# Optimization experiments

Hardware: AMD Instinct MI355X
Metric: run time of the kernel (lower is better)

## Reference

```python
import jax, jax.numpy as jnp
import numpy as np

B = 8           # hardcoded batchsize in the original forward
EPS = 1e-4      # scn.BatchNormalization default eps


def setup_inputs() -> dict:
    key = jax.random.key(0)
    ks = jax.random.split(key, 8)
    Nq, Nkv = 16384, 32768
    dec_in, enc_in, nf = 64, 64, 128
    nbr = jax.random.randint(ks[2], (Nq, 27), 0, Nq, dtype=jnp.int32)
    # center tap of the 3x3x3 submanifold conv is the point itself
    nbr = nbr.at[:, 13].set(jnp.arange(Nq, dtype=jnp.int32))
    return {
        "x_decoder_feat": jax.random.normal(ks[0], (Nq, dec_in), jnp.float32),
        "x_encoder_feat": jax.random.normal(ks[1], (Nkv, enc_in), jnp.float32),
        "nbr_idx": nbr,
        "W_p1": jax.random.normal(ks[3], (27, dec_in, nf), jnp.float32) * 0.05,
        "W_q": jax.random.normal(ks[4], (nf, nf), jnp.float32) * 0.05,
        "W_k": jax.random.normal(ks[5], (enc_in, nf), jnp.float32) * 0.05,
        "W_v": jax.random.normal(ks[6], (enc_in, nf), jnp.float32) * 0.05,
        "W_trans": jax.random.normal(ks[7], (nf, nf), jnp.float32) * 0.05,
        "gamma": jnp.ones((nf,), jnp.float32),
        "beta": jnp.zeros((nf,), jnp.float32),
    }


def reference(x_decoder_feat, x_encoder_feat, nbr_idx, W_p1, W_q, W_k, W_v,
              W_trans, gamma, beta):
    nf = W_q.shape[1]
    # p1: 3x3x3 submanifold conv = gather 27 neighbors, per-offset matmul, sum
    x_dec = jnp.einsum('nkc,kcf->nf', x_decoder_feat[nbr_idx], W_p1)  # [Nq,nf]
    q = (x_dec @ W_q).reshape(B, -1, nf)            # [B, nq, nf]
    k = (x_encoder_feat @ W_k).reshape(B, -1, nf)   # [B, nkv, nf]
    v = (x_encoder_feat @ W_v).reshape(B, -1, nf)
    # per-batch QK^T softmax V (no 1/sqrt(d) scaling in original)
    attn = jax.nn.softmax(jnp.einsum('bqc,bkc->bqk', q, k), axis=-1)
    x_r = jnp.einsum('bqk,bkc->bqc', attn, v).reshape(-1, nf)  # [Nq,nf]
    # trans_conv (1x1) + batchnorm (batch stats over all points)
    t = x_r @ W_trans
    mean = t.mean(axis=0)
    var = t.var(axis=0)
    bn = (t - mean) * jax.lax.rsqrt(var + EPS) * gamma + beta
    return x_dec + bn
```

## Files before the change

### kernel.cpp

```cpp
#include <hip/hip_runtime.h>
#include <math.h>

#define NQ      16384
#define NKV     32768
#define CIN     64
#define NF      128
#define NOFF    27
#define BATCH   8
#define SQ      2048
#define SKV     4096
#define BN_EPS  1e-4f
#define SPLIT   4
#define KV_PER_SPLIT (SKV / SPLIT)
#define TILES_PER_SPLIT (KV_PER_SPLIT / 64)
#define LOG2E   1.4426950408889634f
#define SHIFT2  57.70780163555854f

typedef unsigned short u16;
typedef unsigned int   u32;
typedef __attribute__((ext_vector_type(4))) float f32x4;
typedef __attribute__((ext_vector_type(8))) short s16x8;

__device__ __forceinline__ u16 f2b(float x) {
    union { float f; unsigned u; } c; c.f = x;
    unsigned r = (c.u + 0x7FFFu + ((c.u >> 16) & 1u)) >> 16;
    return (u16)r;
}
__device__ __forceinline__ float b2f(u16 x) {
    union { unsigned u; float f; } c; c.u = ((unsigned)x) << 16;
    return c.f;
}
__device__ __forceinline__ u32 pk2bf(float lo, float hi) {
    union { float f; u32 u; } a, b;
    a.f = lo; b.f = hi;
    return __builtin_amdgcn_perm(b.u + 0x8000u, a.u + 0x8000u, 0x07060302u);
}
__device__ __forceinline__ void g2l16(const void* gp, void* lp) {
    __builtin_amdgcn_global_load_lds(
        (const __attribute__((address_space(1))) unsigned*)gp,
        (__attribute__((address_space(3))) unsigned*)lp, 16, 0, 0);
}

__device__ __forceinline__ void wtrans_one(
    const float* __restrict__ src, u16* __restrict__ dst, int K, int id, float sc)
{
    int n  = id / (K / 4);
    int k4 = (id % (K / 4)) * 4;
    const float* s = src + (size_t)k4 * NF + n;
    ushort4 o;
    o.x = f2b(s[0] * sc); o.y = f2b(s[NF] * sc);
    o.z = f2b(s[2 * NF] * sc); o.w = f2b(s[3 * NF] * sc);
    *(ushort4*)(dst + (size_t)n * K + k4) = o;
}

__global__ __launch_bounds__(256) void prep_kernel(
    const float* __restrict__ xdec_feat, const float* __restrict__ Wp1,
    const float* __restrict__ Wq, const float* __restrict__ Wk,
    const float* __restrict__ Wv, const float* __restrict__ Wt,
    u16* __restrict__ xf_bf, u16* __restrict__ wp1t,
    u16* __restrict__ wqT, u16* __restrict__ wkT,
    u16* __restrict__ wvT, u16* __restrict__ wtT,
    float* __restrict__ stats)
{
    int bid = blockIdx.x;
    int t   = threadIdx.x;
    if (bid < 1024) {
        int i = (bid * 256 + t) * 4;
        float4 v = *(const float4*)(xdec_feat + i);
        ushort4 o;
        o.x = f2b(v.x); o.y = f2b(v.y); o.z = f2b(v.z); o.w = f2b(v.w);
        *(ushort4*)(xf_bf + i) = o;
    } else if (bid < 1240) {
        int id = (bid - 1024) * 256 + t;
        int ko = id >> 11;
        int r  = id & 2047;
        int f  = r >> 4;
        int c4 = (r & 15) * 4;
        const float* s = Wp1 + (size_t)ko * 8192 + (size_t)c4 * NF + f;
        ushort4 o;
        o.x = f2b(s[0]); o.y = f2b(s[NF]); o.z = f2b(s[2 * NF]); o.w = f2b(s[3 * NF]);
        *(ushort4*)(wp1t + (size_t)ko * 8192 + (size_t)f * 64 + c4) = o;
    } else if (bid < 1288) {
        int id = (bid - 1240) * 256 + t;
        if (id < 4096)        wtrans_one(Wq, wqT, 128, id, LOG2E);
        else if (id < 6144)   wtrans_one(Wk, wkT, 64, id - 4096, 1.f);
        else if (id < 8192)   wtrans_one(Wv, wvT, 64, id - 6144, 1.f);
        else                  wtrans_one(Wt, wtT, 128, id - 8192, 1.f);
    } else {
        stats[t] = 0.f;
    }
}

__global__ __launch_bounds__(256) void main_fused_kernel(
    const float* __restrict__ xenc, const u16* __restrict__ xf,
    const int* __restrict__ nbr, const u16* __restrict__ wp1t,
    const u16* __restrict__ wqT, const u16* __restrict__ wkT,
    const u16* __restrict__ wvT,
    u16* __restrict__ kbuf, u16* __restrict__ vt,
    float* __restrict__ xdec, u16* __restrict__ qbuf)
{
    __shared__ u16 Bs[2][128][64];
    __shared__ int nbr_s[64][28];

    const int t    = threadIdx.x;
    const int w    = t >> 6;
    const int lane = t & 63;
    const int quad = lane >> 4;
    const int l15  = lane & 15;

    if (blockIdx.x < 512) {
        const int m0 = blockIdx.x * 64 + w * 16;
        const float* Ap = xenc + (size_t)(m0 + l15) * CIN + quad * 8;
        float4 a0 = *(const float4*)(Ap);
        float4 a1 = *(const float4*)(Ap + 4);
        float4 a2 = *(const float4*)(Ap + 32);
        float4 a3 = *(const float4*)(Ap + 36);
        union { u16 a[8]; s16x8 v; } p0, p1;
        p0.a[0] = f2b(a0.x); p0.a[1] = f2b(a0.y); p0.a[2] = f2b(a0.z); p0.a[3] = f2b(a0.w);
        p0.a[4] = f2b(a1.x); p0.a[5] = f2b(a1.y); p0.a[6] = f2b(a1.z); p0.a[7] = f2b(a1.w);
        p1.a[0] = f2b(a2.x); p1.a[1] = f2b(a2.y); p1.a[2] = f2b(a2.z); p1.a[3] = f2b(a2.w);
        p1.a[4] = f2b(a3.x); p1.a[5] = f2b(a3.y); p1.a[6] = f2b(a3.z); p1.a[7] = f2b(a3.w);
        s16x8 af0 = p0.v, af1 = p1.v;

        int m  = m0 + quad * 4;
        int bb = m >> 12;
        int kv = m & 4095;
        #pragma unroll
        for (int nt = 0; nt < 8; nt++) {
            f32x4 ka = (f32x4)0.f, va = (f32x4)0.f;
            const u16* Kp = wkT + (size_t)(nt * 16 + l15) * CIN + quad * 8;
            const u16* Vp = wvT + (size_t)(nt * 16 + l15) * CIN + quad * 8;
            s16x8 kb0 = *(const s16x8*)(Kp);
            s16x8 kb1 = *(const s16x8*)(Kp + 32);
            s16x8 vb0 = *(const s16x8*)(Vp);
            s16x8 vb1 = *(const s16x8*)(Vp + 32);
            ka = __builtin_amdgcn_mfma_f32_16x16x32_bf16(af0, kb0, ka, 0, 0, 0);
            ka = __builtin_amdgcn_mfma_f32_16x16x32_bf16(af1, kb1, ka, 0, 0, 0);
            va = __builtin_amdgcn_mfma_f32_16x16x32_bf16(af0, vb0, va, 0, 0, 0);
            va = __builtin_amdgcn_mfma_f32_16x16x32_bf16(af1, vb1, va, 0, 0, 0);
            #pragma unroll
            for (int r = 0; r < 4; r++)
                kbuf[(size_t)(m0 + quad * 4 + r) * NF + nt * 16 + l15] = f2b(ka[r]);
            ushort4 pk;
            pk.x = f2b(va[0]); pk.y = f2b(va[1]); pk.z = f2b(va[2]); pk.w = f2b(va[3]);
            *(ushort4*)(vt + (size_t)(bb * NF + nt * 16 + l15) * SKV + kv) = pk;
        }
        return;
    }

    const int base = (blockIdx.x - 512) * 64;

    for (int i = t; i < 64 * NOFF; i += 256)
        nbr_s[i / NOFF][i % NOFF] = nbr[(size_t)base * NOFF + i];

    f32x4 oacc[8];
    #pragma unroll
    for (int n = 0; n < 8; n++) oacc[n] = (f32x4)0.f;

    const int arow = w * 16 + l15;
    const int sr   = w * 32 + (lane >> 3);

    #pragma unroll
    for (int c = 0; c < 4; c++) {
        int row = sr + c * 8;
        int kk  = (lane & 7) ^ (row & 7);
        g2l16(wp1t + (size_t)row * 64 + kk * 8, &Bs[0][w * 32 + c * 8][0]);
    }
    __syncthreads();

    for (int ko = 0; ko < NOFF; ko++) {
        int cur = ko & 1;
        if (ko + 1 < NOFF) {
            int nxt = (ko + 1) & 1;
            #pragma unroll
            for (int c = 0; c < 4; c++) {
                int row = sr + c * 8;
                int kk  = (lane & 7) ^ (row & 7);
                g2l16(wp1t + (size_t)(ko + 1) * 8192 + (size_t)row * 64 + kk * 8,
                      &Bs[nxt][w * 32 + c * 8][0]);
            }
        }
        int nb = nbr_s[arow][ko];
        const u16* ap = xf + (size_t)nb * CIN + quad * 8;
        s16x8 af0 = *(const s16x8*)(ap);
        s16x8 af1 = *(const s16x8*)(ap + 32);
        #pragma unroll
        for (int nt = 0; nt < 8; nt++) {
            int pc0 = quad ^ (l15 & 7);
            int pc1 = (4 + quad) ^ (l15 & 7);
            s16x8 bf0 = *(const s16x8*)&Bs[cur][nt * 16 + l15][pc0 * 8];
            s16x8 bf1 = *(const s16x8*)&Bs[cur][nt * 16 + l15][pc1 * 8];
            oacc[nt] = __builtin_amdgcn_mfma_f32_16x16x32_bf16(af0, bf0, oacc[nt], 0, 0, 0);
            oacc[nt] = __builtin_amdgcn_mfma_f32_16x16x32_bf16(af1, bf1, oacc[nt], 0, 0, 0);
        }
        __syncthreads();
    }

    u16* xq = &Bs[0][0][0];
    #pragma unroll
    for (int nt = 0; nt < 8; nt++)
        #pragma unroll
        for (int r = 0; r < 4; r++) {
            int row = w * 16 + quad * 4 + r;
            int col = nt * 16 + l15;
            xdec[(size_t)(base + row) * NF + col] = oacc[nt][r];
            xq[row * 136 + col] = f2b(oacc[nt][r]);
        }

    s16x8 aq[4];
    #pragma unroll
    for (int ks = 0; ks < 4; ks++)
        aq[ks] = *(const s16x8*)&xq[(w * 16 + l15) * 136 + ks * 32 + quad * 8];

    #pragma unroll
    for (int nt = 0; nt < 8; nt++) {
        f32x4 acc = (f32x4)0.f;
        const u16* Wp = wqT + (size_t)(nt * 16 + l15) * NF + quad * 8;
        #pragma unroll
        for (int ks = 0; ks < 4; ks++) {
            s16x8 bf = *(const s16x8*)(Wp + ks * 32);
            acc = __builtin_amdgcn_mfma_f32_16x16x32_bf16(aq[ks], bf, acc, 0, 0, 0);
        }
        #pragma unroll
        for (int r = 0; r < 4; r++)
            qbuf[(size_t)(base + w * 16 + quad * 4 + r) * NF + nt * 16 + l15] = f2b(acc[r]);
    }
}

__global__ __launch_bounds__(256) void attn_mfma_kernel(
    const u16* __restrict__ Q, const u16* __restrict__ K,
    const u16* __restrict__ Vt, u16* __restrict__ Opart,
    float* __restrict__ lpart)
{
    __shared__ u16 Ks[2][64][128];
    __shared__ u16 Vs[2][128][64];
    __shared__ u16 Ps[4][16][72];

    const int t    = threadIdx.x;
    const int b    = blockIdx.y;
    const int q0   = blockIdx.x * 128;
    const int sp   = blockIdx.z;
    const int w    = t >> 6;
    const int lane = t & 63;
    const int quad = lane >> 4;
    const int l15  = lane & 15;

    const u16* Kb  = K  + (size_t)b * SKV * NF;
    const u16* Vtb = Vt + (size_t)b * NF * SKV;

    s16x8 qf[2][4];
    #pragma unroll
    for (int g = 0; g < 2; g++) {
        const u16* Qp = Q + ((size_t)(b * SQ + q0 + w * 32 + g * 16 + l15)) * NF + quad * 8;
        #pragma unroll
        for (int ks = 0; ks < 4; ks++) qf[g][ks] = *(const s16x8*)(Qp + ks * 32);
    }

    f32x4 oacc[2][8];
    #pragma unroll
    for (int g = 0; g < 2; g++)
        #pragma unroll
        for (int n = 0; n < 8; n++) oacc[g][n] = (f32x4)0.f;
    float lrow[2] = {0.f, 0.f};

    const int kvbase = sp * KV_PER_SPLIT;
    const int krow = w * 16 + (lane >> 4);
    const int vrow = w * 32 + (lane >> 3);

    #pragma unroll
    for (int c = 0; c < 4; c++) {
        int row = krow + c * 4;
        int k8  = (lane & 15) ^ (row & 15);
        g2l16(Kb + (size_t)(kvbase + row) * NF + k8 * 8, &Ks[0][w * 16 + c * 4][0]);
    }
    #pragma unroll
    for (int c = 0; c < 4; c++) {
        int row = vrow + c * 8;
        int k8  = (lane & 7) ^ (row & 7);
        g2l16(Vtb + (size_t)row * SKV + kvbase + k8 * 8, &Vs[0][w * 32 + c * 8][0]);
    }

    for (int tile = 0; tile < TILES_PER_SPLIT; tile++) {
        const int cur = tile & 1;
        __syncthreads();
        if (tile + 1 < TILES_PER_SPLIT) {
            const int nxt = (tile + 1) & 1;
            int kvn = kvbase + (tile + 1) * 64;
            #pragma unroll
            for (int c = 0; c < 4; c++) {
                int row = krow + c * 4;
                int k8  = (lane & 15) ^ (row & 15);
                g2l16(Kb + (size_t)(kvn + row) * NF + k8 * 8, &Ks[nxt][w * 16 + c * 4][0]);
            }
            #pragma unroll
            for (int c = 0; c < 4; c++) {
                int row = vrow + c * 8;
                int k8  = (lane & 7) ^ (row & 7);
                g2l16(Vtb + (size_t)row * SKV + kvn + k8 * 8, &Vs[nxt][w * 32 + c * 8][0]);
            }
        }

        f32x4 sacc[2][4];
        #pragma unroll
        for (int c = 0; c < 4; c++) {
            sacc[0][c] = (f32x4)0.f;
            sacc[1][c] = (f32x4)0.f;
            #pragma unroll
            for (int ks = 0; ks < 4; ks++) {
                int p = (ks * 4 + quad) ^ l15;
                s16x8 ka = *(const s16x8*)&Ks[cur][c * 16 + l15][p * 8];
                sacc[0][c] = __builtin_amdgcn_mfma_f32_16x16x32_bf16(ka, qf[0][ks], sacc[0][c], 0, 0, 0);
                sacc[1][c] = __builtin_amdgcn_mfma_f32_16x16x32_bf16(ka, qf[1][ks], sacc[1][c], 0, 0, 0);
            }
        }

        s16x8 pb[2][2];
        #pragma unroll
        for (int g = 0; g < 2; g++) {
            float rs = 0.f;
            float pv[4][4];
            #pragma unroll
            for (int c = 0; c < 4; c++)
                #pragma unroll
                for (int r = 0; r < 4; r++) {
                    float p = exp2f(sacc[g][c][r] - SHIFT2);
                    pv[c][r] = p;
                    rs += p;
                }
            rs += __shfl_xor(rs, 16);
            rs += __shfl_xor(rs, 32);
            lrow[g] += rs;
            #pragma unroll
            for (int c = 0; c < 4; c++) {
                uint2 pk;
                pk.x = pk2bf(pv[c][0], pv[c][1]);
                pk.y = pk2bf(pv[c][2], pv[c][3]);
                *(uint2*)&Ps[w][l15][c * 16 + quad * 4] = pk;
            }
            pb[g][0] = *(const s16x8*)&Ps[w][l15][quad * 8];
            pb[g][1] = *(const s16x8*)&Ps[w][l15][32 + quad * 8];
        }

        #pragma unroll
        for (int mt = 0; mt < 8; mt++) {
            int p0 = quad ^ (l15 & 7);
            int p1 = (4 + quad) ^ (l15 & 7);
            s16x8 va0 = *(const s16x8*)&Vs[cur][mt * 16 + l15][p0 * 8];
            s16x8 va1 = *(const s16x8*)&Vs[cur][mt * 16 + l15][p1 * 8];
            oacc[0][mt] = __builtin_amdgcn_mfma_f32_16x16x32_bf16(va0, pb[0][0], oacc[0][mt], 0, 0, 0);
            oacc[0][mt] = __builtin_amdgcn_mfma_f32_16x16x32_bf16(va1, pb[0][1], oacc[0][mt], 0, 0, 0);
            oacc[1][mt] = __builtin_amdgcn_mfma_f32_16x16x32_bf16(va0, pb[1][0], oacc[1][mt], 0, 0, 0);
            oacc[1][mt] = __builtin_amdgcn_mfma_f32_16x16x32_bf16(va1, pb[1][1], oacc[1][mt], 0, 0, 0);
        }
    }

    #pragma unroll
    for (int g = 0; g < 2; g++) {
        int grow = b * SQ + q0 + w * 32 + g * 16 + l15;
        u16* Ob = Opart + (size_t)sp * NQ * NF + (size_t)grow * NF;
        #pragma unroll
        for (int mt = 0; mt < 8; mt++) {
            uint2 ov;
            ov.x = pk2bf(oacc[g][mt][0], oacc[g][mt][1]);
            ov.y = pk2bf(oacc[g][mt][2], oacc[g][mt][3]);
            *(uint2*)(Ob + mt * 16 + quad * 4) = ov;
        }
        if (quad == 0) lpart[sp * NQ + grow] = lrow[g];
    }
}

__global__ __launch_bounds__(256) void tgemm_fused_kernel(
    const u16* __restrict__ Opart, const float* __restrict__ lpart,
    const u16* __restrict__ WT, float* __restrict__ C, float* __restrict__ stats)
{
    const int t    = threadIdx.x;
    const int w    = t >> 6;
    const int lane = t & 63;
    const int quad = lane >> 4;
    const int l15  = lane & 15;
    const int m0   = blockIdx.x * 64 + w * 16;
    const int row  = m0 + l15;

    float L = 0.f;
    #pragma unroll
    for (int s = 0; s < SPLIT; s++) L += lpart[s * NQ + row];
    float invL = 1.f / L;

    s16x8 af[4];
    #pragma unroll
    for (int ks = 0; ks < 4; ks++) {
        float sum[8] = {0.f, 0.f, 0.f, 0.f, 0.f, 0.f, 0.f, 0.f};
        #pragma unroll
        for (int s = 0; s < SPLIT; s++) {
            const u16* p = Opart + (size_t)s * NQ * NF + (size_t)row * NF + ks * 32 + quad * 8;
            ushort4 u0 = *(const ushort4*)p;
            ushort4 u1 = *(const ushort4*)(p + 4);
            sum[0] += b2f(u0.x); sum[1] += b2f(u0.y);
            sum[2] += b2f(u0.z); sum[3] += b2f(u0.w);
            sum[4] += b2f(u1.x); sum[5] += b2f(u1.y);
            sum[6] += b2f(u1.z); sum[7] += b2f(u1.w);
        }
        union { u16 a[8]; s16x8 v; } pk;
        #pragma unroll
        for (int j = 0; j < 8; j++) pk.a[j] = f2b(sum[j] * invL);
        af[ks] = pk.v;
    }

    f32x4 oacc[8];
    #pragma unroll
    for (int nt = 0; nt < 8; nt++) {
        oacc[nt] = (f32x4)0.f;
        const u16* Wp = WT + (size_t)(nt * 16 + l15) * NF + quad * 8;
        #pragma unroll
        for (int ks = 0; ks < 4; ks++) {
            s16x8 bf = *(const s16x8*)(Wp + ks * 32);
            oacc[nt] = __builtin_amdgcn_mfma_f32_16x16x32_bf16(af[ks], bf, oacc[nt], 0, 0, 0);
        }
    }

    float s[8], sq[8];
    #pragma unroll
    for (int nt = 0; nt < 8; nt++) {
        s[nt] = 0.f; sq[nt] = 0.f;
        #pragma unroll
        for (int r = 0; r < 4; r++) {
            float v = oacc[nt][r];
            C[(size_t)(m0 + quad * 4 + r) * NF + nt * 16 + l15] = v;
            s[nt] += v; sq[nt] += v * v;
        }
    }
    #pragma unroll
    for (int nt = 0; nt < 8; nt++) {
        s[nt]  += __shfl_xor(s[nt], 16);  s[nt]  += __shfl_xor(s[nt], 32);
        sq[nt] += __shfl_xor(sq[nt], 16); sq[nt] += __shfl_xor(sq[nt], 32);
    }
    __shared__ float red[2][4][128];
    if (quad == 0) {
        #pragma unroll
        for (int nt = 0; nt < 8; nt++) {
            red[0][w][nt * 16 + l15] = s[nt];
            red[1][w][nt * 16 + l15] = sq[nt];
        }
    }
    __syncthreads();
    if (t < 128) {
        float a = red[0][0][t] + red[0][1][t] + red[0][2][t] + red[0][3][t];
        atomicAdd(&stats[t], a);
    } else if (t < 256) {
        int f = t - 128;
        float a = red[1][0][f] + red[1][1][f] + red[1][2][f] + red[1][3][f];
        atomicAdd(&stats[128 + f], a);
    }
}

__global__ __launch_bounds__(256) void bn_finalize(
    const float* __restrict__ tbuf, const float* __restrict__ xdec,
    const float* __restrict__ stats, const float* __restrict__ gamma,
    const float* __restrict__ beta, float* __restrict__ out)
{
    const int g = blockIdx.x * 256 + threadIdx.x;
    const int e = g * 4;
    const int f = e & (NF - 1);
    const float invN = 1.0f / (float)NQ;
    float4 tv = *(const float4*)(tbuf + e);
    float4 xv = *(const float4*)(xdec + e);
    float o[4], tt[4] = {tv.x, tv.y, tv.z, tv.w}, xx[4] = {xv.x, xv.y, xv.z, xv.w};
    #pragma unroll
    for (int u = 0; u < 4; u++) {
        float sum  = stats[f + u];
        float sumq = stats[128 + f + u];
        float mean = sum * invN;
        float var  = sumq * invN - mean * mean;
        float sc   = rsqrtf(var + BN_EPS) * gamma[f + u];
        o[u] = xx[u] + (tt[u] - mean) * sc + beta[f + u];
    }
    float4 ov = make_float4(o[0], o[1], o[2], o[3]);
    *(float4*)(out + e) = ov;
}

extern "C" void kernel_launch(void* const* d_in, const int* in_sizes, int n_in,
                              void* d_out, int out_size, void* d_ws, size_t ws_size,
                              hipStream_t stream) {
    const float* xdec_feat = (const float*)d_in[0];
    const float* xenc_feat = (const float*)d_in[1];
    const int*   nbr       = (const int*)d_in[2];
    const float* Wp1       = (const float*)d_in[3];
    const float* Wq        = (const float*)d_in[4];
    const float* Wk        = (const float*)d_in[5];
    const float* Wv        = (const float*)d_in[6];
    const float* Wt        = (const float*)d_in[7];
    const float* gamma     = (const float*)d_in[8];
    const float* beta      = (const float*)d_in[9];
    float* out = (float*)d_out;

    char* wsb = (char*)d_ws;
    const size_t MB = 1024 * 1024;
    float* xdec   = (float*)(wsb + 0);
    u16*   qbuf   = (u16*)  (wsb + 8 * MB);
    u16*   kbuf   = (u16*)  (wsb + 12 * MB);
    u16*   vt     = (u16*)  (wsb + 20 * MB);
    u16*   opart  = (u16*)  (wsb + 28 * MB);
    u16*   xf_bf  = (u16*)  (wsb + 44 * MB);
    u16*   wp1t   = (u16*)  (wsb + 46 * MB);
    u16*   wqT    = (u16*)  (wsb + 46 * MB + 512 * 1024);
    u16*   wkT    = (u16*)  (wsb + 46 * MB + 512 * 1024 + 32768);
    u16*   wvT    = (u16*)  (wsb + 46 * MB + 512 * 1024 + 49152);
    u16*   wtT    = (u16*)  (wsb + 46 * MB + 512 * 1024 + 65536);
    float* lpart  = (float*)(wsb + 47 * MB);
    float* stats  = (float*)(wsb + 47 * MB + 512 * 1024);
    float* tbuf   = (float*)(wsb + 12 * MB);

    prep_kernel<<<1289, 256, 0, stream>>>(
        xdec_feat, Wp1, Wq, Wk, Wv, Wt,
        xf_bf, wp1t, wqT, wkT, wvT, wtT, stats);
    main_fused_kernel<<<768, 256, 0, stream>>>(
        xenc_feat, xf_bf, nbr, wp1t, wqT, wkT, wvT,
        kbuf, vt, xdec, qbuf);
    attn_mfma_kernel<<<dim3(SQ / 128, BATCH, SPLIT), 256, 0, stream>>>(
        qbuf, kbuf, vt, opart, lpart);
    tgemm_fused_kernel<<<NQ / 64, 256, 0, stream>>>(opart, lpart, wtT, tbuf, stats);
    bn_finalize<<<(NQ * NF) / 1024, 256, 0, stream>>>(tbuf, xdec, stats, gamma, beta, out);
}
```

Measured before the change: 194.6 us.

## Stage V-transpose through LDS, prefetch gathered rows, split tgemm over columns

Three separate changes. The K/V projection now writes V tiles into shared memory and then stores them to the transposed buffer as coalesced 16-byte rows, where before each lane did a scattered 8-byte store. The neighbor-gather conv loads the next offset's feature row one iteration ahead so the gather latency overlaps with the MFMAs. The output-projection GEMM is split across two column halves via a 2D grid, which doubles block count but has each half re-read and re-reduce the attention partials.

Measured after the change: 200.7 us. 1.03x slower.

```diff
diff --git a/kernel.cpp b/kernel.cpp
--- a/kernel.cpp
+++ b/kernel.cpp
@@ -99,7 +99,7 @@
     u16* __restrict__ kbuf, u16* __restrict__ vt,
     float* __restrict__ xdec, u16* __restrict__ qbuf)
 {
-    __shared__ u16 Bs[2][128][64];
+    __shared__ u16 smem[2][128][64];
     __shared__ int nbr_s[64][28];
 
     const int t    = threadIdx.x;
@@ -109,7 +109,8 @@
     const int l15  = lane & 15;
 
     if (blockIdx.x < 512) {
-        const int m0 = blockIdx.x * 64 + w * 16;
+        const int bm0 = blockIdx.x * 64;
+        const int m0  = bm0 + w * 16;
         const float* Ap = xenc + (size_t)(m0 + l15) * CIN + quad * 8;
         float4 a0 = *(const float4*)(Ap);
         float4 a1 = *(const float4*)(Ap + 4);
@@ -122,9 +123,7 @@
         p1.a[4] = f2b(a3.x); p1.a[5] = f2b(a3.y); p1.a[6] = f2b(a3.z); p1.a[7] = f2b(a3.w);
         s16x8 af0 = p0.v, af1 = p1.v;
 
-        int m  = m0 + quad * 4;
-        int bb = m >> 12;
-        int kv = m & 4095;
+        u16* vtile = &smem[0][0][0];
         #pragma unroll
         for (int nt = 0; nt < 8; nt++) {
             f32x4 ka = (f32x4)0.f, va = (f32x4)0.f;
@@ -143,7 +142,18 @@
                 kbuf[(size_t)(m0 + quad * 4 + r) * NF + nt * 16 + l15] = f2b(ka[r]);
             ushort4 pk;
             pk.x = f2b(va[0]); pk.y = f2b(va[1]); pk.z = f2b(va[2]); pk.w = f2b(va[3]);
-            *(ushort4*)(vt + (size_t)(bb * NF + nt * 16 + l15) * SKV + kv) = pk;
+            *(ushort4*)&vtile[(nt * 16 + l15) * 64 + w * 16 + quad * 4] = pk;
+        }
+        __syncthreads();
+        int bb  = bm0 >> 12;
+        int kv0 = bm0 & 4095;
+        #pragma unroll
+        for (int it = 0; it < 4; it++) {
+            int idx = it * 256 + t;
+            int row = idx >> 3;
+            int ch  = idx & 7;
+            *(uint4*)(vt + (size_t)(bb * NF + row) * SKV + kv0 + ch * 8) =
+                *(const uint4*)&vtile[row * 64 + ch * 8];
         }
         return;
     }
@@ -164,12 +174,17 @@
     for (int c = 0; c < 4; c++) {
         int row = sr + c * 8;
         int kk  = (lane & 7) ^ (row & 7);
-        g2l16(wp1t + (size_t)row * 64 + kk * 8, &Bs[0][w * 32 + c * 8][0]);
+        g2l16(wp1t + (size_t)row * 64 + kk * 8, &smem[0][w * 32 + c * 8][0]);
     }
     __syncthreads();
+
+    int nb0 = nbr_s[arow][0];
+    s16x8 af0 = *(const s16x8*)(xf + (size_t)nb0 * CIN + quad * 8);
+    s16x8 af1 = *(const s16x8*)(xf + (size_t)nb0 * CIN + quad * 8 + 32);
 
     for (int ko = 0; ko < NOFF; ko++) {
         int cur = ko & 1;
+        s16x8 nf0, nf1;
         if (ko + 1 < NOFF) {
             int nxt = (ko + 1) & 1;
             #pragma unroll
@@ -177,26 +192,27 @@
                 int row = sr + c * 8;
                 int kk  = (lane & 7) ^ (row & 7);
                 g2l16(wp1t + (size_t)(ko + 1) * 8192 + (size_t)row * 64 + kk * 8,
-                      &Bs[nxt][w * 32 + c * 8][0]);
+                      &smem[nxt][w * 32 + c * 8][0]);
             }
-        }
-        int nb = nbr_s[arow][ko];
-        const u16* ap = xf + (size_t)nb * CIN + quad * 8;
-        s16x8 af0 = *(const s16x8*)(ap);
-        s16x8 af1 = *(const s16x8*)(ap + 32);
+            int nb = nbr_s[arow][ko + 1];
+            nf0 = *(const s16x8*)(xf + (size_t)nb * CIN + quad * 8);
+            nf1 = *(const s16x8*)(xf + (size_t)nb * CIN + quad * 8 + 32);
+        }
         #pragma unroll
         for (int nt = 0; nt < 8; nt++) {
             int pc0 = quad ^ (l15 & 7);
             int pc1 = (4 + quad) ^ (l15 & 7);
-            s16x8 bf0 = *(const s16x8*)&Bs[cur][nt * 16 + l15][pc0 * 8];
-            s16x8 bf1 = *(const s16x8*)&Bs[cur][nt * 16 + l15][pc1 * 8];
+            s16x8 bf0 = *(const s16x8*)&smem[cur][nt * 16 + l15][pc0 * 8];
+            s16x8 bf1 = *(const s16x8*)&smem[cur][nt * 16 + l15][pc1 * 8];
             oacc[nt] = __builtin_amdgcn_mfma_f32_16x16x32_bf16(af0, bf0, oacc[nt], 0, 0, 0);
             oacc[nt] = __builtin_amdgcn_mfma_f32_16x16x32_bf16(af1, bf1, oacc[nt], 0, 0, 0);
         }
+        af0 = nf0;
+        af1 = nf1;
         __syncthreads();
     }
 
-    u16* xq = &Bs[0][0][0];
+    u16* xq = &smem[0][0][0];
     #pragma unroll
     for (int nt = 0; nt < 8; nt++)
         #pragma unroll
@@ -380,6 +396,7 @@
     const int l15  = lane & 15;
     const int m0   = blockIdx.x * 64 + w * 16;
     const int row  = m0 + l15;
+    const int ny   = blockIdx.y;
 
     float L = 0.f;
     #pragma unroll
@@ -406,11 +423,11 @@
         af[ks] = pk.v;
     }
 
-    f32x4 oacc[8];
-    #pragma unroll
-    for (int nt = 0; nt < 8; nt++) {
+    f32x4 oacc[4];
+    #pragma unroll
+    for (int nt = 0; nt < 4; nt++) {
         oacc[nt] = (f32x4)0.f;
-        const u16* Wp = WT + (size_t)(nt * 16 + l15) * NF + quad * 8;
+        const u16* Wp = WT + (size_t)(ny * 64 + nt * 16 + l15) * NF + quad * 8;
         #pragma unroll
         for (int ks = 0; ks < 4; ks++) {
             s16x8 bf = *(const s16x8*)(Wp + ks * 32);
@@ -418,38 +435,38 @@
         }
     }
 
-    float s[8], sq[8];
-    #pragma unroll
-    for (int nt = 0; nt < 8; nt++) {
+    float s[4], sq[4];
+    #pragma unroll
+    for (int nt = 0; nt < 4; nt++) {
         s[nt] = 0.f; sq[nt] = 0.f;
         #pragma unroll
         for (int r = 0; r < 4; r++) {
             float v = oacc[nt][r];
-            C[(size_t)(m0 + quad * 4 + r) * NF + nt * 16 + l15] = v;
+            C[(size_t)(m0 + quad * 4 + r) * NF + ny * 64 + nt * 16 + l15] = v;
             s[nt] += v; sq[nt] += v * v;
         }
     }
     #pragma unroll
-    for (int nt = 0; nt < 8; nt++) {
+    for (int nt = 0; nt < 4; nt++) {
         s[nt]  += __shfl_xor(s[nt], 16);  s[nt]  += __shfl_xor(s[nt], 32);
         sq[nt] += __shfl_xor(sq[nt], 16); sq[nt] += __shfl_xor(sq[nt], 32);
     }
-    __shared__ float red[2][4][128];
+    __shared__ float red[2][4][64];
     if (quad == 0) {
         #pragma unroll
-        for (int nt = 0; nt < 8; nt++) {
+        for (int nt = 0; nt < 4; nt++) {
             red[0][w][nt * 16 + l15] = s[nt];
             red[1][w][nt * 16 + l15] = sq[nt];
         }
     }
     __syncthreads();
-    if (t < 128) {
+    if (t < 64) {
         float a = red[0][0][t] + red[0][1][t] + red[0][2][t] + red[0][3][t];
-        atomicAdd(&stats[t], a);
-    } else if (t < 256) {
-        int f = t - 128;
+        atomicAdd(&stats[ny * 64 + t], a);
+    } else if (t < 128) {
+        int f = t - 64;
         float a = red[1][0][f] + red[1][1][f] + red[1][2][f] + red[1][3][f];
-        atomicAdd(&stats[128 + f], a);
+        atomicAdd(&stats[128 + ny * 64 + f], a);
     }
 }
 
@@ -518,6 +535,6 @@
         kbuf, vt, xdec, qbuf);
     attn_mfma_kernel<<<dim3(SQ / 128, BATCH, SPLIT), 256, 0, stream>>>(
         qbuf, kbuf, vt, opart, lpart);
-    tgemm_fused_kernel<<<NQ / 64, 256, 0, stream>>>(opart, lpart, wtT, tbuf, stats);
+    tgemm_fused_kernel<<<dim3(NQ / 64, 2), 256, 0, stream>>>(opart, lpart, wtT, tbuf, stats);
     bn_finalize<<<(NQ * NF) / 1024, 256, 0, stream>>>(tbuf, xdec, stats, gamma, beta, out);
 }
```
